# Kernel optimization log

Measured on AMD Instinct MI355X. Metric: run time of the kernel, lower is better.

## Reference

```python
import jax, jax.numpy as jnp
import numpy as np
from jax import lax

B = 512
THRESHOLD = 0.5
CFG = [64, 64, 'M', 128, 128, 'M', 256, 256, 256, 'M', 512, 512, 512, 'M', 512, 512, 512, 'M']  # VGG16


def _conv_relu(x, w, b):
    # x: [B,C,H,W], w: [O,I,3,3] (torch OIHW layout), pad=1 stride=1
    y = lax.conv_general_dilated(x, w, (1, 1), 'SAME',
                                 dimension_numbers=('NCHW', 'OIHW', 'NCHW'))
    return jax.nn.relu(y + b[None, :, None, None])


def _maxpool2(x):
    return lax.reduce_window(x, -jnp.inf, lax.max, (1, 1, 2, 2), (1, 1, 2, 2), 'VALID')


def _features(x, ws, bs):
    i = 0
    for c in CFG:
        if c == 'M':
            x = _maxpool2(x)
        else:
            x = _conv_relu(x, ws[i], bs[i])
            i += 1
    return x  # [B,512,1,1]


def _gcn(distance):
    # Faithful translation, including the source bug: 'onetensor' is zeros_like,
    # so mask==0 everywhere and A_hat collapses to the identity.
    n = distance.shape[0]
    zero = jnp.zeros_like(distance)
    one = jnp.zeros_like(distance)  # bug in original: torch.zeros_like for onetensor
    adj = jnp.where(distance > THRESHOLD, distance, zero)
    mask = jnp.where(distance > THRESHOLD, one, zero)
    idx = lax.top_k(adj, 10)[1]                                   # [n,10]
    top10 = jnp.zeros_like(adj).at[jnp.arange(n)[:, None], idx].set(1.0)
    top10 = top10 * mask
    a_hat = top10 + jnp.eye(n, dtype=distance.dtype)
    d_inv = jnp.diag(1.0 / jnp.sum(a_hat, axis=1))
    return lax.stop_gradient(a_hat @ d_inv)                        # [n,n]


def _forward(x, target, conv_ws, conv_bs, lin1_w, lin1_b, lin2_w, lin2_b, cls_w, cls_b):
    feat = _features(x, conv_ws, conv_bs).reshape(x.shape[0], -1)  # [B,512]
    h = jax.nn.relu(feat @ lin1_w + lin1_b)                        # [B,256]
    low = h @ lin2_w + lin2_b                                      # [B,128]
    graph_pre = jax.nn.sigmoid(low @ low.T)                        # [B,B]
    graph_gt = (target[:, None] == target[None, :]).astype(jnp.float32)
    mat = _gcn(graph_pre)                                          # [B,B], detached
    out = (mat @ feat) @ cls_w + cls_b                             # [B,10]
    return out, graph_pre, graph_gt


def setup_inputs() -> dict:
    key = jax.random.key(0)
    ks = iter(jax.random.split(key, 64))
    inp = {}
    inp['x'] = jax.random.normal(next(ks), (B, 3, 32, 32), dtype=jnp.float32)
    inp['target'] = jax.random.randint(next(ks), (B,), 0, 10)
    in_c, i = 3, 0
    for c in CFG:
        if c == 'M':
            continue
        scale = 1.0 / np.sqrt(in_c * 9.0)
        inp['conv%d_w' % i] = jax.random.normal(next(ks), (c, in_c, 3, 3), dtype=jnp.float32) * scale
        inp['conv%d_b' % i] = jnp.zeros((c,), dtype=jnp.float32)
        in_c, i = c, i + 1
    inp['lin1_w'] = jax.random.normal(next(ks), (512, 256), dtype=jnp.float32) * (1.0 / np.sqrt(512.0))
    inp['lin1_b'] = jnp.zeros((256,), dtype=jnp.float32)
    inp['lin2_w'] = jax.random.normal(next(ks), (256, 128), dtype=jnp.float32) * (1.0 / np.sqrt(256.0))
    inp['lin2_b'] = jnp.zeros((128,), dtype=jnp.float32)
    inp['cls_w'] = jax.random.normal(next(ks), (512, 10), dtype=jnp.float32) * (1.0 / np.sqrt(512.0))
    inp['cls_b'] = jnp.zeros((10,), dtype=jnp.float32)
    return inp


def reference(x, target,
              conv0_w, conv0_b, conv1_w, conv1_b, conv2_w, conv2_b, conv3_w, conv3_b,
              conv4_w, conv4_b, conv5_w, conv5_b, conv6_w, conv6_b, conv7_w, conv7_b,
              conv8_w, conv8_b, conv9_w, conv9_b, conv10_w, conv10_b, conv11_w, conv11_b,
              conv12_w, conv12_b,
              lin1_w, lin1_b, lin2_w, lin2_b, cls_w, cls_b):
    ws = [conv0_w, conv1_w, conv2_w, conv3_w, conv4_w, conv5_w, conv6_w,
          conv7_w, conv8_w, conv9_w, conv10_w, conv11_w, conv12_w]
    bs = [conv0_b, conv1_b, conv2_b, conv3_b, conv4_b, conv5_b, conv6_b,
          conv7_b, conv8_b, conv9_b, conv10_b, conv11_b, conv12_b]
    return _forward(x, target, ws, bs, lin1_w, lin1_b, lin2_w, lin2_b, cls_w, cls_b)
```

## Files before the change

kernel.cpp:

```cpp
#include <hip/hip_runtime.h>

typedef unsigned short u16;
typedef __bf16 bf16x8 __attribute__((ext_vector_type(8)));
typedef float floatx4 __attribute__((ext_vector_type(4)));

__device__ inline u16 f2bf(float f) {
    return __builtin_bit_cast(u16, (__bf16)f);
}
__device__ inline float bf2f(u16 h) {
    return __uint_as_float(((unsigned int)h) << 16);
}

__device__ __forceinline__ void async_copy16(u16* lds, const u16* g) {
    __builtin_amdgcn_global_load_lds(
        (const __attribute__((address_space(1))) unsigned int*)(uintptr_t)g,
        (__attribute__((address_space(3))) unsigned int*)(unsigned int)(uintptr_t)lds,
        16, 0, 0);
}

__global__ void zero_halo(u16* __restrict__ buf, int Hp, int C, int total8)
{
    int i = blockIdx.x * 256 + threadIdx.x;
    if (i >= total8) return;
    int c8 = i % (C / 8);
    int p  = i / (C / 8);
    int ring = 4 * Hp - 4;
    int h = p % ring;
    int b = p / ring;
    int y, x;
    if (h < Hp)              { y = 0;              x = h; }
    else if (h < 2 * Hp)     { y = Hp - 1;         x = h - Hp; }
    else if (h < 3 * Hp - 2) { y = h - 2 * Hp + 1; x = 0; }
    else                     { y = h - 3 * Hp + 3; x = Hp - 1; }
    uint4 z = make_uint4(0u, 0u, 0u, 0u);
    *(uint4*)(buf + ((size_t)((b * Hp + y) * Hp + x) * C) + c8 * 8) = z;
}

__global__ __launch_bounds__(256) void conv0_mfma(
    const float* __restrict__ x, const float* __restrict__ w,
    const float* __restrict__ bias, u16* __restrict__ out)
{
    __shared__ __align__(16) float xsf[3 * 10 * 36];
    __shared__ int tab[32];
    const int t  = threadIdx.x;
    const int b  = blockIdx.x >> 2;
    const int y0 = (blockIdx.x & 3) * 8;

    for (int i = t; i < 3 * 10 * 36; i += 256) {
        int ci  = i / 360;
        int rem = i % 360;
        int r   = rem / 36;
        int c   = rem % 36;
        int gy  = y0 - 1 + r;
        int gx  = c - 1;
        float v = 0.f;
        if ((unsigned)gy < 32u && (unsigned)gx < 32u)
            v = x[((b * 3 + ci) * 32 + gy) * 32 + gx];
        xsf[i] = v;
    }
    if (t < 32) {
        int k = t, off = 0;
        if (k < 27) {
            int ci = k / 9;
            int r9 = k - ci * 9;
            int rr = r9 / 3;
            int cc = r9 - rr * 3;
            off = (ci * 10 + rr) * 36 + cc;
        }
        tab[t] = off;
    }

    const int lane = t & 63;
    const int wv   = t >> 6;
    const int quad = lane >> 4;
    const int l16  = lane & 15;
    const int q8   = quad * 8;

    bf16x8 bf[4];
    #pragma unroll
    for (int nt = 0; nt < 4; nt++) {
        int col = nt * 16 + l16;
        u16 hh[8];
        #pragma unroll
        for (int j = 0; j < 8; j++) {
            int k = q8 + j;
            float wv_ = (k < 27) ? w[col * 27 + k] : 0.f;
            hh[j] = f2bf(wv_);
        }
        #pragma unroll
        for (int j = 0; j < 8; j++) ((u16*)&bf[nt])[j] = hh[j];
    }
    float bzv[4];
    #pragma unroll
    for (int nt = 0; nt < 4; nt++) bzv[nt] = bias[nt * 16 + l16];

    __syncthreads();

    int tb_[8];
    #pragma unroll
    for (int j = 0; j < 8; j++) tb_[j] = tab[q8 + j];

    bf16x8 af[4];
    #pragma unroll
    for (int mt = 0; mt < 4; mt++) {
        int dm   = wv * 64 + mt * 16 + l16;
        int yloc = dm >> 5;
        int xx   = dm & 31;
        int bix  = yloc * 36 + xx;
        u16 hh[8];
        #pragma unroll
        for (int j = 0; j < 8; j++) hh[j] = f2bf(xsf[bix + tb_[j]]);
        if (quad == 3) {
            #pragma unroll
            for (int j = 3; j < 8; j++) hh[j] = 0;
        }
        #pragma unroll
        for (int j = 0; j < 8; j++) ((u16*)&af[mt])[j] = hh[j];
    }

    floatx4 acc[4][4];
    #pragma unroll
    for (int i = 0; i < 4; i++)
        #pragma unroll
        for (int j = 0; j < 4; j++)
            acc[i][j] = (floatx4){0.f, 0.f, 0.f, 0.f};

    #pragma unroll
    for (int mt = 0; mt < 4; mt++)
        #pragma unroll
        for (int nt = 0; nt < 4; nt++)
            acc[mt][nt] = __builtin_amdgcn_mfma_f32_16x16x32_bf16(
                af[mt], bf[nt], acc[mt][nt], 0, 0, 0);

    #pragma unroll
    for (int mt = 0; mt < 4; mt++) {
        #pragma unroll
        for (int r = 0; r < 4; r++) {
            int p  = wv * 64 + mt * 16 + quad * 4 + r;
            int y  = y0 + (p >> 5);
            int xx = p & 31;
            u16* op = out + (size_t)((b * 34 + y + 1) * 34 + xx + 1) * 64 + l16;
            #pragma unroll
            for (int nt = 0; nt < 4; nt++)
                op[nt * 16] = f2bf(fmaxf(acc[mt][nt][r] + bzv[nt], 0.f));
        }
    }
}

struct RepackArgs {
    const float* src[14];
    u16* dst[14];
    int p1[14];
    int p2[14];
    int startBlk[15];
    int nseg;
};

__global__ __launch_bounds__(256) void repack_all(RepackArgs a)
{
    __shared__ __align__(16) u16 lds[9216];
    int blk = blockIdx.x;
    int s = 0;
    #pragma unroll 1
    while (s + 1 < a.nseg && blk >= a.startBlk[s + 1]) s++;
    const int cb = blk - a.startBlk[s];
    const int t  = threadIdx.x;

    if (a.p2[s] == 0) {
        const int Cin = a.p1[s];
        const int logCin = __builtin_ctz(Cin);
        const float* src = a.src[s] + (size_t)cb * 9216;
        u16* dst = a.dst[s] + (size_t)cb * 9216;
        #pragma unroll
        for (int it = 0; it < 9; it++) {
            int j4 = it * 256 + t;
            float4 v = *(const float4*)(src + j4 * 4);
            ushort4 h;
            h.x = f2bf(v.x); h.y = f2bf(v.y); h.z = f2bf(v.z); h.w = f2bf(v.w);
            *(ushort4*)(lds + j4 * 4) = h;
        }
        __syncthreads();
        #pragma unroll
        for (int it = 0; it < 9; it++) {
            int o4   = (it * 256 + t) * 4;
            int ci   = o4 & (Cin - 1);
            int rest = o4 >> logCin;
            int co   = rest / 9;
            int sh   = rest - co * 9;
            int sb   = (co << logCin) * 9 + ci * 9 + sh;
            ushort4 h;
            h.x = lds[sb]; h.y = lds[sb + 9]; h.z = lds[sb + 18]; h.w = lds[sb + 27];
            *(ushort4*)(dst + o4) = h;
        }
    } else {
        const int K = a.p1[s], N = a.p2[s];
        const int ntx = N >> 6;
        const int k0 = (cb / ntx) * 64, n0 = (cb % ntx) * 64;
        const float* src = a.src[s];
        u16* dst = a.dst[s];
        const int r = t >> 4, c4 = (t & 15) * 4;
        #pragma unroll
        for (int rr = 0; rr < 64; rr += 16) {
            float4 v = *(const float4*)(src + (size_t)(k0 + r + rr) * N + n0 + c4);
            u16* p = lds + (r + rr) * 72 + c4;
            p[0] = f2bf(v.x); p[1] = f2bf(v.y); p[2] = f2bf(v.z); p[3] = f2bf(v.w);
        }
        __syncthreads();
        #pragma unroll
        for (int it = 0; it < 2; it++) {
            int ov = it * 256 + t;
            int n  = ov >> 3;
            int kq = (ov & 7) * 8;
            __align__(16) u16 h[8];
            #pragma unroll
            for (int j = 0; j < 8; j++) h[j] = lds[(kq + j) * 72 + n];
            *(uint4*)(dst + (size_t)(n0 + n) * K + k0 + kq) = *(uint4*)h;
        }
    }
}

template <int BM, int BN>
__global__ __launch_bounds__(256) void conv_gemm(
    const u16* __restrict__ in, const u16* __restrict__ wt,
    const float* __restrict__ bias, u16* __restrict__ out,
    float* __restrict__ partial, size_t pstride,
    int H, int Cin, int Cout, int logHW, int logW, int splitN,
    int outPad, int poolMode)
{
    constexpr int BK = 64;
    constexpr int WC = (BM == 256) ? BN : (BN / 2);
    constexpr int NT = WC / 16;
    constexpr int NB_A = BM / 32;
    constexpr int NB_B = BN / 32;
    constexpr int ASZ = BM * BK;
    constexpr int BSZ = BN * BK;
    __shared__ u16 As[2 * ASZ];
    __shared__ u16 Bs[2 * BSZ];

    const int Nblocks = Cout / BN;
    const int per = gridDim.x >> 3;
    const int bid = (blockIdx.x & 7) * per + (blockIdx.x >> 3);
    const int sp   = bid % splitN;
    const int tile = bid / splitN;
    const int m0 = (tile / Nblocks) * BM;
    const int n0 = (tile % Nblocks) * BN;

    const int t    = threadIdx.x;
    const int lane = t & 63;
    const int wave = t >> 6;
    const int quad = lane >> 4;
    const int l16  = lane & 15;
    const int wm   = (BM == 256) ? wave : (wave >> 1);
    const int wn   = (BM == 256) ? 0 : (wave & 1);
    const int W    = H;
    const int Wp   = H + 2;
    const int HW   = 1 << logHW;
    const int col8 = t & 7;
    const int r0   = t >> 3;
    const int scol = col8 ^ (r0 & 7);

    const int CinB = Cin * 2;

    int vA[NB_A];
    #pragma unroll
    for (int j = 0; j < NB_A; j++) {
        int m  = m0 + r0 + 32 * j;
        int b  = m >> logHW;
        int rm = m & (HW - 1);
        int y  = rm >> logW;
        int xx = rm & (W - 1);
        vA[j] = ((b * Wp + y + 1) * Wp + xx + 1) * CinB + scol * 16;
    }
    int vB[NB_B];
    #pragma unroll
    for (int j = 0; j < NB_B; j++)
        vB[j] = (n0 + r0 + 32 * j) * 9 * CinB + scol * 16;

    const int logKB = (Cin == 64) ? 0 : (Cin == 128) ? 1 : (Cin == 256) ? 2 : 3;
    const int KB  = 1 << logKB;
    const int T   = 9 * KB;
    const int len = T / splitN;
    const int it0 = sp * len;

    int s0 = it0 >> logKB;
    int c3 = s0 - (s0 / 3) * 3;
    int ta = ((s0 / 3 - 1) * Wp + (c3 - 1)) * CinB;
    int kb = (it0 & (KB - 1)) * 128;
    int tb = it0 * 128;

    const char* const inB = (const char*)in;
    const char* const wtB = (const char*)wt;

    floatx4 acc[4][NT];
    #pragma unroll
    for (int i = 0; i < 4; i++)
        #pragma unroll
        for (int j = 0; j < NT; j++)
            acc[i][j] = (floatx4){0.f, 0.f, 0.f, 0.f};

    const int sw = (l16 & 7) * 8;

    auto stage = [&](int ua, int tbv, int buf) {
        u16* la = As + buf * ASZ + t * 8;
        u16* lb = Bs + buf * BSZ + t * 8;
        #pragma unroll
        for (int j = 0; j < NB_A; j++)
            async_copy16(la + j * 2048, (const u16*)(inB + (ua + vA[j])));
        #pragma unroll
        for (int j = 0; j < NB_B; j++)
            async_copy16(lb + j * 2048, (const u16*)(wtB + (tbv + vB[j])));
    };
    auto advance = [&]() {
        tb += 128;
        kb += 128;
        if (kb == CinB) {
            kb = 0;
            ta += (c3 == 2) ? (Wp - 2) * CinB : CinB;
            c3 = (c3 == 2) ? 0 : c3 + 1;
        }
    };

    stage(ta + kb, tb, 0);
    advance();
    __syncthreads();

    int cur = 0;
    for (int it = 0; it < len; it++) {
        if (it + 1 < len) {
            stage(ta + kb, tb, cur ^ 1);
            advance();
        }
        const u16* Ab = As + cur * ASZ;
        const u16* Bb = Bs + cur * BSZ;
        #pragma unroll
        for (int kk = 0; kk < BK; kk += 32) {
            bf16x8 af[4], bfv[NT];
            int cbo = kk + quad * 8;
            #pragma unroll
            for (int mt = 0; mt < 4; mt++)
                af[mt] = *(const bf16x8*)(Ab + (wm * 64 + mt * 16 + l16) * 64 + (cbo ^ sw));
            #pragma unroll
            for (int nt = 0; nt < NT; nt++)
                bfv[nt] = *(const bf16x8*)(Bb + (wn * WC + nt * 16 + l16) * 64 + (cbo ^ sw));
            #pragma unroll
            for (int mt = 0; mt < 4; mt++)
                #pragma unroll
                for (int nt = 0; nt < NT; nt++)
                    acc[mt][nt] = __builtin_amdgcn_mfma_f32_16x16x32_bf16(
                        af[mt], bfv[nt], acc[mt][nt], 0, 0, 0);
        }
        __syncthreads();
        cur ^= 1;
    }

    const int ngb = n0 + wn * WC + l16;

    if (splitN > 1) {
        float* pout = partial + (size_t)sp * pstride;
        #pragma unroll
        for (int mt = 0; mt < 4; mt++)
            #pragma unroll
            for (int r = 0; r < 4; r++) {
                int mg = m0 + wm * 64 + mt * 16 + quad * 4 + r;
                float* op = pout + (size_t)mg * Cout + ngb;
                #pragma unroll
                for (int nt = 0; nt < NT; nt++)
                    op[nt * 16] = acc[mt][nt][r];
            }
        return;
    }

    float bzv[NT];
    #pragma unroll
    for (int nt = 0; nt < NT; nt++) bzv[nt] = bias[ngb + nt * 16];

    if (poolMode) {
        const int Hpo = (H >> 1) + 2;
        if (logW == 5) {
            #pragma unroll
            for (int mt = 0; mt < 2; mt++)
                #pragma unroll
                for (int rp = 0; rp < 2; rp++) {
                    int m1 = m0 + wm * 64 + mt * 16 + quad * 4 + 2 * rp;
                    int b  = m1 >> logHW;
                    int rm = m1 & (HW - 1);
                    int yp = (rm >> logW) >> 1;
                    int xp = (rm & (W - 1)) >> 1;
                    u16* op = out + (size_t)((b * Hpo + yp + 1) * Hpo + xp + 1) * Cout + ngb;
                    #pragma unroll
                    for (int nt = 0; nt < NT; nt++) {
                        float v = fmaxf(
                            fmaxf(acc[mt][nt][2 * rp], acc[mt][nt][2 * rp + 1]),
                            fmaxf(acc[mt + 2][nt][2 * rp], acc[mt + 2][nt][2 * rp + 1]));
                        op[nt * 16] = f2bf(fmaxf(v + bzv[nt], 0.f));
                    }
                }
        } else if (logW == 4) {
            #pragma unroll
            for (int mtp = 0; mtp < 2; mtp++)
                #pragma unroll
                for (int rp = 0; rp < 2; rp++) {
                    int mt = 2 * mtp;
                    int m1 = m0 + wm * 64 + mt * 16 + quad * 4 + 2 * rp;
                    int b  = m1 >> logHW;
                    int rm = m1 & (HW - 1);
                    int yp = (rm >> logW) >> 1;
                    int xp = (rm & (W - 1)) >> 1;
                    u16* op = out + (size_t)((b * Hpo + yp + 1) * Hpo + xp + 1) * Cout + ngb;
                    #pragma unroll
                    for (int nt = 0; nt < NT; nt++) {
                        float v = fmaxf(
                            fmaxf(acc[mt][nt][2 * rp], acc[mt][nt][2 * rp + 1]),
                            fmaxf(acc[mt + 1][nt][2 * rp], acc[mt + 1][nt][2 * rp + 1]));
                        op[nt * 16] = f2bf(fmaxf(v + bzv[nt], 0.f));
                    }
                }
        } else {
            #pragma unroll
            for (int mt = 0; mt < 4; mt++)
                #pragma unroll
                for (int rp = 0; rp < 2; rp++) {
                    int m1 = m0 + wm * 64 + mt * 16 + quad * 4 + 2 * rp;
                    int b  = m1 >> logHW;
                    int rm = m1 & (HW - 1);
                    int yp = (rm >> logW) >> 1;
                    int xp = (rm & (W - 1)) >> 1;
                    u16* op = out + (size_t)((b * Hpo + yp + 1) * Hpo + xp + 1) * Cout + ngb;
                    #pragma unroll
                    for (int nt = 0; nt < NT; nt++) {
                        float a = fmaxf(acc[mt][nt][2 * rp], acc[mt][nt][2 * rp + 1]);
                        float p = __shfl_xor(a, 32, 64);
                        float v = fmaxf(a, p);
                        if (quad < 2)
                            op[nt * 16] = f2bf(fmaxf(v + bzv[nt], 0.f));
                    }
                }
        }
        return;
    }

    #pragma unroll
    for (int mt = 0; mt < 4; mt++) {
        #pragma unroll
        for (int r = 0; r < 4; r++) {
            int mg = m0 + wm * 64 + mt * 16 + quad * 4 + r;
            size_t obase;
            if (outPad) {
                int b  = mg >> logHW;
                int rm = mg & (HW - 1);
                int y  = rm >> logW;
                int xx = rm & (W - 1);
                obase = (size_t)((b * Wp + y + 1) * Wp + xx + 1) * Cout;
            } else {
                obase = (size_t)mg * Cout;
            }
            u16* op = out + obase + ngb;
            #pragma unroll
            for (int nt = 0; nt < NT; nt++)
                op[nt * 16] = f2bf(fmaxf(acc[mt][nt][r] + bzv[nt], 0.f));
        }
    }
}

template <int BM, int BN, int W, int CIN>
__global__ __launch_bounds__(256) void conv_halo(
    const u16* __restrict__ in, const u16* __restrict__ wt,
    const float* __restrict__ bias, u16* __restrict__ out,
    int outPad, int poolMode)
{
    constexpr int BK = 64;
    constexpr int WC = (BM == 256) ? BN : (BN / 2);
    constexpr int NT = WC / 16;
    constexpr int NB_B = BN / 32;
    constexpr int BSZ = BN * BK;
    constexpr int Wp = W + 2;
    constexpr int R  = BM / W;
    constexpr int P  = (R + 2) * Wp;
    constexpr int CinB = CIN * 2;
    constexpr int CH = CinB / 16;
    constexpr int LOG_CH = (CH == 8) ? 3 : 4;
    constexpr int HALO_CHUNKS = P * CH;
    constexpr int ROUNDS = (HALO_CHUNKS + 255) / 256;
    constexpr int logW = (W == 32) ? 5 : 4;
    constexpr int logHW = 2 * logW;
    constexpr int HW = 1 << logHW;
    constexpr int KB = CIN / 64;
    constexpr int T  = 9 * KB;

    __shared__ __align__(16) u16 Ah[P * CH * 8];
    __shared__ __align__(16) u16 Bs[2 * BSZ];

    constexpr int Nblocks = 1;
    static_assert(true, "");
    const int per = gridDim.x >> 3;
    const int bid = (blockIdx.x & 7) * per + (blockIdx.x >> 3);
    const int m0 = (bid / Nblocks) * BM;
    const int n0 = (bid % Nblocks) * BN;

    const int t    = threadIdx.x;
    const int lane = t & 63;
    const int wave = t >> 6;
    const int quad = lane >> 4;
    const int l16  = lane & 15;
    const int wm   = (BM == 256) ? wave : (wave >> 1);
    const int wn   = (BM == 256) ? 0 : (wave & 1);
    const int col8 = t & 7;
    const int r0   = t >> 3;
    const int scol = col8 ^ (r0 & 7);

    const int b  = m0 >> logHW;
    const int y0 = (m0 & (HW - 1)) >> logW;

    const char* hsrc = (const char*)in + (size_t)((b * Wp + y0) * Wp) * CinB;
    #pragma unroll
    for (int rd = 0; rd < ROUNDS; rd++) {
        int i = rd * 256 + t;
        if ((HALO_CHUNKS % 256 == 0) || i < HALO_CHUNKS) {
            int pp   = i >> LOG_CH;
            int si   = i ^ (pp & 7);
            async_copy16(Ah + i * 8, (const u16*)(hsrc + (size_t)si * 16));
        }
    }

    int vB[NB_B];
    #pragma unroll
    for (int j = 0; j < NB_B; j++)
        vB[j] = (n0 + r0 + 32 * j) * 9 * CinB + scol * 16;
    const char* const wtB = (const char*)wt;
    auto stageB = [&](int tbv, int buf) {
        u16* lb = Bs + buf * BSZ + t * 8;
        #pragma unroll
        for (int j = 0; j < NB_B; j++)
            async_copy16(lb + j * 2048, (const u16*)(wtB + (tbv + vB[j])));
    };

    int pBase[4];
    #pragma unroll
    for (int mt = 0; mt < 4; mt++) {
        int dm = wm * 64 + mt * 16 + l16;
        pBase[mt] = (dm >> logW) * Wp + (dm & (W - 1));
    }

    floatx4 acc[4][NT];
    #pragma unroll
    for (int i = 0; i < 4; i++)
        #pragma unroll
        for (int j = 0; j < NT; j++)
            acc[i][j] = (floatx4){0.f, 0.f, 0.f, 0.f};

    const int sw = (l16 & 7) * 8;
    const char* const AhB = (const char*)Ah;

    stageB(0, 0);
    __syncthreads();

    int cur = 0, tb = 128;
    int pOff = 0, c3 = 0, cb = 0;
    for (int it = 0; it < T; it++) {
        if (it + 1 < T) { stageB(tb, cur ^ 1); tb += 128; }
        const int pO = pOff, cbv = cb;
        cb += 128;
        if (cb == CinB) {
            cb = 0;
            pOff += (c3 == 2) ? (Wp - 2) : 1;
            c3 = (c3 == 2) ? 0 : c3 + 1;
        }

        bf16x8 af[2][4];
        #pragma unroll
        for (int mt = 0; mt < 4; mt++) {
            int p  = pBase[mt] + pO;
            int pc = p & 7;
            int ab = p * CinB + cbv;
            #pragma unroll
            for (int kk2 = 0; kk2 < 2; kk2++) {
                int kq = kk2 * 4 + quad;
                af[kk2][mt] = *(const bf16x8*)(AhB + ab + ((kq ^ pc) << 4));
            }
        }

        const u16* Bb = Bs + cur * BSZ;
        #pragma unroll
        for (int kk2 = 0; kk2 < 2; kk2++) {
            int cbo = kk2 * 32 + quad * 8;
            bf16x8 bfv[NT];
            #pragma unroll
            for (int nt = 0; nt < NT; nt++)
                bfv[nt] = *(const bf16x8*)(Bb + (wn * WC + nt * 16 + l16) * 64 + (cbo ^ sw));
            #pragma unroll
            for (int mt = 0; mt < 4; mt++)
                #pragma unroll
                for (int nt = 0; nt < NT; nt++)
                    acc[mt][nt] = __builtin_amdgcn_mfma_f32_16x16x32_bf16(
                        af[kk2][mt], bfv[nt], acc[mt][nt], 0, 0, 0);
        }
        __syncthreads();
        cur ^= 1;
    }

    const int ngb = n0 + wn * WC + l16;
    float bzv[NT];
    #pragma unroll
    for (int nt = 0; nt < NT; nt++) bzv[nt] = bias[ngb + nt * 16];
    const int Cout = BN;
    const int H = W;

    if (poolMode) {
        const int Hpo = (H >> 1) + 2;
        if (logW == 5) {
            #pragma unroll
            for (int mt = 0; mt < 2; mt++)
                #pragma unroll
                for (int rp = 0; rp < 2; rp++) {
                    int m1 = m0 + wm * 64 + mt * 16 + quad * 4 + 2 * rp;
                    int bb = m1 >> logHW;
                    int rm = m1 & (HW - 1);
                    int yp = (rm >> logW) >> 1;
                    int xp = (rm & (W - 1)) >> 1;
                    u16* op = out + (size_t)((bb * Hpo + yp + 1) * Hpo + xp + 1) * Cout + ngb;
                    #pragma unroll
                    for (int nt = 0; nt < NT; nt++) {
                        float v = fmaxf(
                            fmaxf(acc[mt][nt][2 * rp], acc[mt][nt][2 * rp + 1]),
                            fmaxf(acc[mt + 2][nt][2 * rp], acc[mt + 2][nt][2 * rp + 1]));
                        op[nt * 16] = f2bf(fmaxf(v + bzv[nt], 0.f));
                    }
                }
        } else {
            #pragma unroll
            for (int mtp = 0; mtp < 2; mtp++)
                #pragma unroll
                for (int rp = 0; rp < 2; rp++) {
                    int mt = 2 * mtp;
                    int m1 = m0 + wm * 64 + mt * 16 + quad * 4 + 2 * rp;
                    int bb = m1 >> logHW;
                    int rm = m1 & (HW - 1);
                    int yp = (rm >> logW) >> 1;
                    int xp = (rm & (W - 1)) >> 1;
                    u16* op = out + (size_t)((bb * Hpo + yp + 1) * Hpo + xp + 1) * Cout + ngb;
                    #pragma unroll
                    for (int nt = 0; nt < NT; nt++) {
                        float v = fmaxf(
                            fmaxf(acc[mt][nt][2 * rp], acc[mt][nt][2 * rp + 1]),
                            fmaxf(acc[mt + 1][nt][2 * rp], acc[mt + 1][nt][2 * rp + 1]));
                        op[nt * 16] = f2bf(fmaxf(v + bzv[nt], 0.f));
                    }
                }
        }
        return;
    }

    #pragma unroll
    for (int mt = 0; mt < 4; mt++) {
        #pragma unroll
        for (int r = 0; r < 4; r++) {
            int mg = m0 + wm * 64 + mt * 16 + quad * 4 + r;
            size_t obase;
            if (outPad) {
                int bb = mg >> logHW;
                int rm = mg & (HW - 1);
                int y  = rm >> logW;
                int xx = rm & (W - 1);
                obase = (size_t)((bb * Wp + y + 1) * Wp + xx + 1) * Cout;
            } else {
                obase = (size_t)mg * Cout;
            }
            u16* op = out + obase + ngb;
            #pragma unroll
            for (int nt = 0; nt < NT; nt++)
                op[nt * 16] = f2bf(fmaxf(acc[mt][nt][r] + bzv[nt], 0.f));
        }
    }
}

__global__ void reduce_split(const float* __restrict__ partial,
                             const float* __restrict__ bias, u16* __restrict__ out,
                             int MN, int C, int logC, int splitN, size_t pstride,
                             int H, int logHW, int logW, int outPad)
{
    int i4 = (blockIdx.x * 256 + threadIdx.x) * 4;
    if (i4 >= MN) return;
    float4 s = *(const float4*)(partial + i4);
    for (int sp = 1; sp < splitN; sp++) {
        float4 p = *(const float4*)(partial + (size_t)sp * pstride + i4);
        s.x += p.x; s.y += p.y; s.z += p.z; s.w += p.w;
    }
    int n = i4 & (C - 1);
    int m = i4 >> logC;
    size_t obase;
    if (outPad) {
        int Wp = H + 2;
        int b  = m >> logHW;
        int rm = m & ((1 << logHW) - 1);
        int y  = rm >> logW;
        int xx = rm & (H - 1);
        obase = (size_t)((b * Wp + y + 1) * Wp + xx + 1) * C;
    } else {
        obase = (size_t)m * C;
    }
    ushort4 o;
    o.x = f2bf(fmaxf(s.x + bias[n + 0], 0.f));
    o.y = f2bf(fmaxf(s.y + bias[n + 1], 0.f));
    o.z = f2bf(fmaxf(s.z + bias[n + 2], 0.f));
    o.w = f2bf(fmaxf(s.w + bias[n + 3], 0.f));
    *(ushort4*)(out + obase + n) = o;
}

__global__ void reduce_pool(const float* __restrict__ partial,
                            const float* __restrict__ bias, u16* __restrict__ out,
                            int total4, int C, int splitN, size_t pstride,
                            int H, int outPad)
{
    int idx = blockIdx.x * 256 + threadIdx.x;
    if (idx >= total4) return;
    int c4 = idx % (C / 4);
    int p  = idx / (C / 4);
    int Ho = H >> 1;
    int xp = p % Ho; p /= Ho;
    int yp = p % Ho;
    int b  = p / Ho;
    int n  = c4 * 4;
    float4 best;
    bool first = true;
    #pragma unroll
    for (int dy = 0; dy < 2; dy++)
        #pragma unroll
        for (int dx = 0; dx < 2; dx++) {
            int m = (b * H + 2 * yp + dy) * H + 2 * xp + dx;
            const float* q = partial + (size_t)m * C + n;
            float4 s = *(const float4*)q;
            for (int sp = 1; sp < splitN; sp++) {
                float4 pp = *(const float4*)(q + (size_t)sp * pstride);
                s.x += pp.x; s.y += pp.y; s.z += pp.z; s.w += pp.w;
            }
            if (first) { best = s; first = false; }
            else {
                best.x = fmaxf(best.x, s.x); best.y = fmaxf(best.y, s.y);
                best.z = fmaxf(best.z, s.z); best.w = fmaxf(best.w, s.w);
            }
        }
    size_t obase;
    if (outPad) {
        int Hpo = Ho + 2;
        obase = (size_t)((b * Hpo + yp + 1) * Hpo + xp + 1) * C;
    } else {
        obase = (size_t)((b * Ho + yp) * Ho + xp) * C;
    }
    ushort4 o;
    o.x = f2bf(fmaxf(best.x + bias[n + 0], 0.f));
    o.y = f2bf(fmaxf(best.y + bias[n + 1], 0.f));
    o.z = f2bf(fmaxf(best.z + bias[n + 2], 0.f));
    o.w = f2bf(fmaxf(best.w + bias[n + 3], 0.f));
    *(ushort4*)(out + obase + n) = o;
}

template <bool RELU, bool OUTBF>
__global__ __launch_bounds__(256) void gemm64(
    const u16* __restrict__ A, const u16* __restrict__ Bt,
    const float* __restrict__ bias, void* __restrict__ outv,
    int M, int N, int K)
{
    constexpr int LDP = 72;
    __shared__ u16 As[64 * LDP];
    __shared__ u16 Bs[64 * LDP];

    const int nb = N >> 6;
    const int m0 = (blockIdx.x / nb) * 64;
    const int n0 = (blockIdx.x % nb) * 64;
    const int t = threadIdx.x, lane = t & 63, wave = t >> 6;
    const int quad = lane >> 4, l16 = lane & 15;
    const int wm = wave >> 1, wn = wave & 1;
    const int col8 = t & 7, r0 = t >> 3;

    floatx4 acc[2][2];
    #pragma unroll
    for (int i = 0; i < 2; i++)
        #pragma unroll
        for (int j = 0; j < 2; j++)
            acc[i][j] = (floatx4){0.f, 0.f, 0.f, 0.f};

    for (int kb = 0; kb < K; kb += 64) {
        #pragma unroll
        for (int j = 0; j < 2; j++) {
            int row = r0 + 32 * j;
            *(uint4*)(As + row * LDP + col8 * 8) =
                *(const uint4*)(A + (size_t)(m0 + row) * K + kb + col8 * 8);
            *(uint4*)(Bs + row * LDP + col8 * 8) =
                *(const uint4*)(Bt + (size_t)(n0 + row) * K + kb + col8 * 8);
        }
        __syncthreads();
        #pragma unroll
        for (int kk = 0; kk < 64; kk += 32) {
            bf16x8 af[2], bfv[2];
            #pragma unroll
            for (int mt = 0; mt < 2; mt++)
                af[mt] = *(const bf16x8*)(As + (wm * 32 + mt * 16 + l16) * LDP + kk + quad * 8);
            #pragma unroll
            for (int nt = 0; nt < 2; nt++)
                bfv[nt] = *(const bf16x8*)(Bs + (wn * 32 + nt * 16 + l16) * LDP + kk + quad * 8);
            #pragma unroll
            for (int mt = 0; mt < 2; mt++)
                #pragma unroll
                for (int nt = 0; nt < 2; nt++)
                    acc[mt][nt] = __builtin_amdgcn_mfma_f32_16x16x32_bf16(
                        af[mt], bfv[nt], acc[mt][nt], 0, 0, 0);
        }
        __syncthreads();
    }
    #pragma unroll
    for (int mt = 0; mt < 2; mt++) {
        #pragma unroll
        for (int nt = 0; nt < 2; nt++) {
            #pragma unroll
            for (int r = 0; r < 4; r++) {
                int mg = m0 + wm * 32 + mt * 16 + quad * 4 + r;
                int ng = n0 + wn * 32 + nt * 16 + l16;
                float v = acc[mt][nt][r] + bias[ng];
                if (RELU) v = fmaxf(v, 0.f);
                if (OUTBF) ((u16*)outv)[(size_t)mg * N + ng] = f2bf(v);
                else       ((float*)outv)[(size_t)mg * N + ng] = v;
            }
        }
    }
}

__global__ __launch_bounds__(256) void graph_tile(
    const float* __restrict__ low, const int* __restrict__ target,
    float* __restrict__ gpre, float* __restrict__ ggt)
{
    __shared__ float Al[64 * 132];
    __shared__ float Bl[128 * 68];
    const int t = threadIdx.x;
    const int gr0 = (blockIdx.x >> 3) * 64;
    const int gc0 = (blockIdx.x & 7) * 64;

    #pragma unroll
    for (int j = 0; j < 32; j++) {
        int flat = t + 256 * j;
        int k = flat & 127;
        int rc = flat >> 7;
        Al[rc * 132 + k] = low[(size_t)(gr0 + rc) * 128 + k];
        Bl[k * 68 + rc]  = low[(size_t)(gc0 + rc) * 128 + k];
    }
    __syncthreads();

    const int tx = t & 15, ty = t >> 4;
    float acc[4][4];
    #pragma unroll
    for (int r = 0; r < 4; r++)
        #pragma unroll
        for (int c = 0; c < 4; c++) acc[r][c] = 0.f;

    for (int k = 0; k < 128; k++) {
        float a[4], b[4];
        #pragma unroll
        for (int r = 0; r < 4; r++) a[r] = Al[(ty * 4 + r) * 132 + k];
        #pragma unroll
        for (int c = 0; c < 4; c++) b[c] = Bl[k * 68 + tx * 4 + c];
        #pragma unroll
        for (int r = 0; r < 4; r++)
            #pragma unroll
            for (int c = 0; c < 4; c++) acc[r][c] += a[r] * b[c];
    }
    #pragma unroll
    for (int r = 0; r < 4; r++) {
        int row = gr0 + ty * 4 + r;
        int tr  = target[row];
        float4 gp, gg;
        float* pp = (float*)&gp;
        float* gg_ = (float*)&gg;
        #pragma unroll
        for (int c = 0; c < 4; c++) {
            pp[c]  = 1.f / (1.f + __expf(-acc[r][c]));
            gg_[c] = (tr == target[gc0 + tx * 4 + c]) ? 1.f : 0.f;
        }
        *(float4*)(gpre + (size_t)row * 512 + gc0 + tx * 4) = gp;
        *(float4*)(ggt  + (size_t)row * 512 + gc0 + tx * 4) = gg;
    }
}

__global__ __launch_bounds__(256) void cls_kernel(
    const u16* __restrict__ feat, const float* __restrict__ w,
    const float* __restrict__ bias, float* __restrict__ out)
{
    __shared__ float ws[5120];
    const int t = threadIdx.x;
    for (int i = t; i < 5120; i += 256) ws[i] = w[i];
    __syncthreads();
    const int lane = t & 63;
    const int row  = blockIdx.x * 4 + (t >> 6);
    float a[10];
    #pragma unroll
    for (int j = 0; j < 10; j++) a[j] = 0.f;
    #pragma unroll
    for (int i = 0; i < 8; i++) {
        int k = i * 64 + lane;
        float f = bf2f(feat[(size_t)row * 512 + k]);
        #pragma unroll
        for (int j = 0; j < 10; j++) a[j] += f * ws[k * 10 + j];
    }
    #pragma unroll
    for (int j = 0; j < 10; j++)
        #pragma unroll
        for (int off = 32; off > 0; off >>= 1)
            a[j] += __shfl_down(a[j], off, 64);
    if (lane == 0) {
        #pragma unroll
        for (int j = 0; j < 10; j++) out[row * 10 + j] = a[j] + bias[j];
    }
}

extern "C" void kernel_launch(void* const* d_in, const int* in_sizes, int n_in,
                              void* d_out, int out_size, void* d_ws, size_t ws_size,
                              hipStream_t stream)
{
    const float* x      = (const float*)d_in[0];
    const int*   target = (const int*)d_in[1];
    const float* conv_w[13];
    const float* conv_b[13];
    for (int i = 0; i < 13; i++) {
        conv_w[i] = (const float*)d_in[2 + 2 * i];
        conv_b[i] = (const float*)d_in[3 + 2 * i];
    }
    const float* lin1_w = (const float*)d_in[28];
    const float* lin1_b = (const float*)d_in[29];
    const float* lin2_w = (const float*)d_in[30];
    const float* lin2_b = (const float*)d_in[31];
    const float* cls_w  = (const float*)d_in[32];
    const float* cls_b  = (const float*)d_in[33];
    float* out = (float*)d_out;

    static const int cin_arr[13]  = {3, 64, 64, 128, 128, 256, 256, 256, 512, 512, 512, 512, 512};
    static const int cout_arr[13] = {64, 64, 128, 128, 256, 256, 256, 512, 512, 512, 512, 512, 512};

    char* ws = (char*)d_ws;
    size_t off = 0;
    const size_t R0SZ = (size_t)512 * 34 * 34 * 64 * 2;
    const size_t R1SZ = (size_t)512 * 34 * 34 * 64 * 2;
    char* R0raw = ws + off; off += R0SZ;
    char* R1raw = ws + off; off += R1SZ;
    u16* R0 = (u16*)R0raw;
    u16* R1 = (u16*)R1raw;
    float* PA = (float*)(R0raw + 20971520);
    float* PB = (float*)(R1raw + 20971520);
    u16* wt[13];
    for (int i = 1; i < 13; i++) {
        wt[i] = (u16*)(ws + off);
        off += (size_t)cout_arr[i] * 9 * cin_arr[i] * 2;
    }
    u16* wtl1 = (u16*)(ws + off); off += (size_t)256 * 512 * 2;
    u16* wtl2 = (u16*)(ws + off); off += (size_t)128 * 256 * 2;
    u16* hbuf = (u16*)(ws + off); off += (size_t)512 * 256 * 2;
    float* lowbuf = (float*)(ws + off); off += (size_t)512 * 128 * 4;

    RepackArgs ra;
    int nb = 0, blk = 0;
    ra.startBlk[0] = 0;
    for (int i = 1; i < 13; i++) {
        ra.src[nb] = conv_w[i];
        ra.dst[nb] = wt[i];
        ra.p1[nb] = cin_arr[i];
        ra.p2[nb] = 0;
        blk += cout_arr[i] * cin_arr[i] / 1024;
        nb++; ra.startBlk[nb] = blk;
    }
    ra.src[nb] = lin1_w; ra.dst[nb] = wtl1; ra.p1[nb] = 512; ra.p2[nb] = 256;
    blk += (512 / 64) * (256 / 64);
    nb++; ra.startBlk[nb] = blk;
    ra.src[nb] = lin2_w; ra.dst[nb] = wtl2; ra.p1[nb] = 256; ra.p2[nb] = 128;
    blk += (256 / 64) * (128 / 64);
    nb++; ra.startBlk[nb] = blk;
    ra.nseg = nb;
    repack_all<<<blk, 256, 0, stream>>>(ra);

    auto zh = [&](u16* buf, int Hp, int C) {
        int total8 = 512 * (4 * Hp - 4) * (C / 8);
        zero_halo<<<(total8 + 255) / 256, 256, 0, stream>>>(buf, Hp, C, total8);
    };
    auto launch_conv = [&](int li, int Hl, int bm, int bn, u16* inb, u16* outb,
                           float* part, int splitN, int outPad, int poolMode) {
        int Cin = cin_arr[li], Cout = cout_arr[li];
        int M = 512 * Hl * Hl;
        int logW = __builtin_ctz(Hl);
        int logHW = 2 * logW;
        size_t pstride = (size_t)M * Cout;
        int grid = (M / bm) * (Cout / bn) * splitN;
        if (bm == 256) {
            conv_gemm<256, 64><<<grid, 256, 0, stream>>>(
                inb, wt[li], conv_b[li], outb, part, pstride,
                Hl, Cin, Cout, logHW, logW, splitN, outPad, poolMode);
        } else if (bn == 128) {
            conv_gemm<128, 128><<<grid, 256, 0, stream>>>(
                inb, wt[li], conv_b[li], outb, part, pstride,
                Hl, Cin, Cout, logHW, logW, splitN, outPad, poolMode);
        } else {
            conv_gemm<128, 64><<<grid, 256, 0, stream>>>(
                inb, wt[li], conv_b[li], outb, part, pstride,
                Hl, Cin, Cout, logHW, logW, splitN, outPad, poolMode);
        }
    };
    auto launch_reduce = [&](int li, int Hl, u16* outb, float* part, int splitN, int outPad) {
        int Cout = cout_arr[li];
        int M = 512 * Hl * Hl;
        int logW = __builtin_ctz(Hl);
        size_t pstride = (size_t)M * Cout;
        int MN = M * Cout;
        reduce_split<<<(MN / 4 + 255) / 256, 256, 0, stream>>>(
            part, conv_b[li], outb, MN, Cout, __builtin_ctz(Cout),
            splitN, pstride, Hl, 2 * logW, logW, outPad);
    };
    auto launch_reduce_pool = [&](int li, int Hl, u16* outb, float* part, int splitN, int outPad) {
        int Cout = cout_arr[li];
        int M = 512 * Hl * Hl;
        size_t pstride = (size_t)M * Cout;
        int total4 = 512 * (Hl / 2) * (Hl / 2) * Cout / 4;
        reduce_pool<<<(total4 + 255) / 256, 256, 0, stream>>>(
            part, conv_b[li], outb, total4, Cout, splitN, pstride, Hl, outPad);
    };

    zh(R0, 34, 64);
    conv0_mfma<<<512 * 4, 256, 0, stream>>>(x, conv_w[0], conv_b[0], R0);

    zh(R1, 18, 64);
    conv_halo<256, 64, 32, 64><<<2048, 256, 0, stream>>>(
        R0, wt[1], conv_b[1], R1, 0, 1);
    zh(R0, 18, 128);
    conv_halo<128, 128, 16, 64><<<1024, 256, 0, stream>>>(
        R1, wt[2], conv_b[2], R0, 1, 0);
    zh(R1, 10, 128);
    conv_halo<128, 128, 16, 128><<<1024, 256, 0, stream>>>(
        R0, wt[3], conv_b[3], R1, 0, 1);
    zh(R0, 10, 256);
    launch_conv(4, 8, 128, 128, R1, R0, nullptr, 1, 1, 0);
    zh(R1, 10, 256);
    launch_conv(5, 8, 128, 128, R0, R1, nullptr, 1, 1, 0);
    zh(R0, 6, 256);
    launch_conv(6, 8, 128, 128, R1, R0, nullptr, 1, 0, 1);
    zh(R1, 6, 512);
    launch_conv(7, 4, 128, 128, R0, R1, PB, 2, 1, 0);
    launch_reduce(7, 4, R1, PB, 2, 1);
    zh(R0, 6, 512);
    launch_conv(8, 4, 128, 128, R1, R0, PA, 2, 1, 0);
    launch_reduce(8, 4, R0, PA, 2, 1);
    zh(R1, 4, 512);
    launch_conv(9, 4, 128, 128, R0, R1, PB, 2, 0, 0);
    launch_reduce_pool(9, 4, R1, PB, 2, 1);
    zh(R0, 4, 512);
    launch_conv(10, 2, 128, 64, R1, R0, PA, 4, 1, 0);
    launch_reduce(10, 2, R0, PA, 4, 1);
    zh(R1, 4, 512);
    launch_conv(11, 2, 128, 64, R0, R1, PB, 4, 1, 0);
    launch_reduce(11, 2, R1, PB, 4, 1);
    launch_conv(12, 2, 128, 64, R1, R0, PA, 4, 0, 0);
    launch_reduce_pool(12, 2, R0, PA, 4, 0);

    u16* feat = R0;
    gemm64<true, true><<<(512 / 64) * (256 / 64), 256, 0, stream>>>(
        feat, wtl1, lin1_b, hbuf, 512, 256, 512);
    gemm64<false, false><<<(512 / 64) * (128 / 64), 256, 0, stream>>>(
        hbuf, wtl2, lin2_b, lowbuf, 512, 128, 256);
    graph_tile<<<64, 256, 0, stream>>>(lowbuf, target, out + 5120, out + 5120 + 262144);
    cls_kernel<<<128, 256, 0, stream>>>(feat, cls_w, cls_b, out);
}
```

Before: 672.8 us.

## Load conv weights directly from global into registers, dropping LDS staging

The halo conv kernel no longer double-buffers weight tiles in shared memory with async copies and per-iteration barriers. Each thread now loads its B fragments straight from global memory (through the cache) into registers every K step, and the __syncthreads in the main loop is removed. This cuts LDS traffic, LDS footprint and barrier stalls. The cost is uncoalesced, latency-exposed global loads with no prefetch overlap and more redundant global reads across waves.

```diff
diff --git a/kernel.cpp b/kernel.cpp
--- a/kernel.cpp
+++ b/kernel.cpp
@@ -468,11 +468,8 @@
     const float* __restrict__ bias, u16* __restrict__ out,
     int outPad, int poolMode)
 {
-    constexpr int BK = 64;
     constexpr int WC = (BM == 256) ? BN : (BN / 2);
     constexpr int NT = WC / 16;
-    constexpr int NB_B = BN / 32;
-    constexpr int BSZ = BN * BK;
     constexpr int Wp = W + 2;
     constexpr int R  = BM / W;
     constexpr int P  = (R + 2) * Wp;
@@ -488,14 +485,11 @@
     constexpr int T  = 9 * KB;
 
     __shared__ __align__(16) u16 Ah[P * CH * 8];
-    __shared__ __align__(16) u16 Bs[2 * BSZ];
-
-    constexpr int Nblocks = 1;
-    static_assert(true, "");
+
     const int per = gridDim.x >> 3;
     const int bid = (blockIdx.x & 7) * per + (blockIdx.x >> 3);
-    const int m0 = (bid / Nblocks) * BM;
-    const int n0 = (bid % Nblocks) * BN;
+    const int m0 = bid * BM;
+    const int n0 = 0;
 
     const int t    = threadIdx.x;
     const int lane = t & 63;
@@ -504,9 +498,6 @@
     const int l16  = lane & 15;
     const int wm   = (BM == 256) ? wave : (wave >> 1);
     const int wn   = (BM == 256) ? 0 : (wave & 1);
-    const int col8 = t & 7;
-    const int r0   = t >> 3;
-    const int scol = col8 ^ (r0 & 7);
 
     const int b  = m0 >> logHW;
     const int y0 = (m0 & (HW - 1)) >> logW;
@@ -522,17 +513,14 @@
         }
     }
 
-    int vB[NB_B];
-    #pragma unroll
-    for (int j = 0; j < NB_B; j++)
-        vB[j] = (n0 + r0 + 32 * j) * 9 * CinB + scol * 16;
+    int vBf[2][NT];
+    #pragma unroll
+    for (int kk2 = 0; kk2 < 2; kk2++)
+        #pragma unroll
+        for (int nt = 0; nt < NT; nt++)
+            vBf[kk2][nt] = (n0 + wn * WC + nt * 16 + l16) * 9 * CinB
+                         + (kk2 * 4 + quad) * 16;
     const char* const wtB = (const char*)wt;
-    auto stageB = [&](int tbv, int buf) {
-        u16* lb = Bs + buf * BSZ + t * 8;
-        #pragma unroll
-        for (int j = 0; j < NB_B; j++)
-            async_copy16(lb + j * 2048, (const u16*)(wtB + (tbv + vB[j])));
-    };
 
     int pBase[4];
     #pragma unroll
@@ -548,16 +536,13 @@
         for (int j = 0; j < NT; j++)
             acc[i][j] = (floatx4){0.f, 0.f, 0.f, 0.f};
 
-    const int sw = (l16 & 7) * 8;
     const char* const AhB = (const char*)Ah;
 
-    stageB(0, 0);
     __syncthreads();
 
-    int cur = 0, tb = 128;
+    int tb = 0;
     int pOff = 0, c3 = 0, cb = 0;
     for (int it = 0; it < T; it++) {
-        if (it + 1 < T) { stageB(tb, cur ^ 1); tb += 128; }
         const int pO = pOff, cbv = cb;
         cb += 128;
         if (cb == CinB) {
@@ -566,6 +551,14 @@
             c3 = (c3 == 2) ? 0 : c3 + 1;
         }
 
+        const char* gb = wtB + tb;
+        bf16x8 bfv[2][NT];
+        #pragma unroll
+        for (int kk2 = 0; kk2 < 2; kk2++)
+            #pragma unroll
+            for (int nt = 0; nt < NT; nt++)
+                bfv[kk2][nt] = *(const bf16x8*)(gb + vBf[kk2][nt]);
+
         bf16x8 af[2][4];
         #pragma unroll
         for (int mt = 0; mt < 4; mt++) {
@@ -579,23 +572,16 @@
             }
         }
 
-        const u16* Bb = Bs + cur * BSZ;
-        #pragma unroll
-        for (int kk2 = 0; kk2 < 2; kk2++) {
-            int cbo = kk2 * 32 + quad * 8;
-            bf16x8 bfv[NT];
-            #pragma unroll
-            for (int nt = 0; nt < NT; nt++)
-                bfv[nt] = *(const bf16x8*)(Bb + (wn * WC + nt * 16 + l16) * 64 + (cbo ^ sw));
+        #pragma unroll
+        for (int kk2 = 0; kk2 < 2; kk2++)
             #pragma unroll
             for (int mt = 0; mt < 4; mt++)
                 #pragma unroll
                 for (int nt = 0; nt < NT; nt++)
                     acc[mt][nt] = __builtin_amdgcn_mfma_f32_16x16x32_bf16(
-                        af[kk2][mt], bfv[nt], acc[mt][nt], 0, 0, 0);
-        }
-        __syncthreads();
-        cur ^= 1;
+                        af[kk2][mt], bfv[kk2][nt], acc[mt][nt], 0, 0, 0);
+
+        tb += 128;
     }
 
     const int ngb = n0 + wn * WC + l16;
```

New measurement: 756.4 us. 12.4% more time.
